# Kernel tuning notes

Hardware: AMD Instinct MI355X
Metric: run time of the kernel (lower is better)

## Reference

```python
import jax, jax.numpy as jnp
import numpy as np

B, N, KS = 4, 4096, 16  # ks = int(k * random_rate) = int(20 * 0.8)
EPS = 1e-5


def bn_relu(x):
    # training-mode BatchNorm (stats over all dims but channel=last) + ReLU
    ax = tuple(range(x.ndim - 1))
    m = x.mean(ax, keepdims=True)
    v = x.var(ax, keepdims=True)
    return jax.nn.relu((x - m) * jax.lax.rsqrt(v + EPS))


def knn_idx(points, ks):
    # points: [B,N,3] -> neighbor indices [B,N,ks] (self included)
    sq = jnp.sum(points * points, -1)
    d2 = sq[:, :, None] + sq[:, None, :] - 2.0 * jnp.einsum('bnd,bmd->bnm', points, points)
    _, idx = jax.lax.top_k(-d2, ks)
    return idx


def gather(f, idx):
    # f: [B,N,C], idx: [B,N,k] -> [B,N,k,C]
    return jax.vmap(lambda ff, ii: ff[ii])(f, idx)


def edge_conv(feat, idx, W, pts=None):
    # EdgeConv: concat(x_i, x_j - x_i [, p_j - p_i]) -> 1x1 conv -> BN+ReLU -> max_k
    nb = gather(feat, idx)                       # [B,N,k,C]
    c = feat[:, :, None, :]
    e = jnp.concatenate([jnp.broadcast_to(c, nb.shape), nb - c], -1)
    if pts is not None:
        e = jnp.concatenate([e, gather(pts, idx) - pts[:, :, None, :]], -1)
    h = jnp.einsum('bnkc,cd->bnkd', e, W)
    return bn_relu(h).max(2)                     # [B,N,out]


def graph_conv(feat, idx, W):
    agg = gather(feat, idx).max(2)               # [B,N,C]
    return bn_relu(agg @ W)


def forward(data, W_fc, b_fc, W1, W2, W3, W4, W5, W6, W10, W11, W12, W13):
    pts = data[..., :3]
    idx = knn_idx(pts, KS)                       # [B,N,KS]
    x0 = bn_relu(data @ W_fc + b_fc)             # fc_start + bn_start, [B,N,64]
    x = edge_conv(x0, idx, W1, pts=pts)          # spFEM 64 -> 256 (edge dim 131)
    x = graph_conv(x, idx, W2)                   # 256 -> 64
    x = graph_conv(x, idx, W3)                   # 64 -> 64
    x1 = x
    x = edge_conv(x, idx, W4)                    # FEM 64 -> 256 (edge dim 128)
    x = graph_conv(x, idx, W5)                   # 256 -> 64
    x = graph_conv(x, idx, W6)                   # 64 -> 64
    x2 = x
    # (conv7..conv90 produce x3/x4 which the head never consumes -> skipped)
    x12 = jnp.concatenate([x1, x2], -1)          # [B,N,128]
    h = bn_relu(x12 @ W10)                       # conv10: 128 -> 1024
    g = h.max(1)                                 # global max pool, [B,1024]
    cat = jnp.concatenate([jnp.broadcast_to(g[:, None, :], (B, N, 1024)), x1, x2], -1)  # [B,N,1152]
    h = bn_relu(cat @ W11)                       # conv11: 1152 -> 512
    h = bn_relu(h @ W12)                         # conv12: 512 -> 256
    out = h @ W13                                # conv13: 256 -> 13 (dropout = identity in eval)
    return out.transpose(0, 2, 1)                # [B,13,N]


def setup_inputs() -> dict:
    key = jax.random.key(0)
    ks = jax.random.split(key, 16)
    w = lambda k, *s: jax.random.normal(k, s, jnp.float32) * 0.05
    return {
        'data': jax.random.normal(ks[0], (B, N, 9), jnp.float32),
        'W_fc': w(ks[1], 9, 64), 'b_fc': jnp.zeros((64,), jnp.float32),
        'W1': w(ks[2], 131, 256),   # 2*64 + 3 (sp variant adds p_j - p_i)
        'W2': w(ks[3], 256, 64), 'W3': w(ks[4], 64, 64),
        'W4': w(ks[5], 128, 256),   # 2*64
        'W5': w(ks[6], 256, 64), 'W6': w(ks[7], 64, 64),
        'W10': w(ks[8], 128, 1024), 'W11': w(ks[9], 1152, 512),
        'W12': w(ks[10], 512, 256), 'W13': w(ks[11], 256, 13),
    }


def reference(data, W_fc, b_fc, W1, W2, W3, W4, W5, W6, W10, W11, W12, W13):
    return forward(data, W_fc, b_fc, W1, W2, W3, W4, W5, W6, W10, W11, W12, W13)
```

## Files before the change

kernel.cpp:

```cpp
#include <hip/hip_runtime.h>
#include <hip/hip_bf16.h>
#include <float.h>

static constexpr int BB  = 4;
static constexpr int NN  = 4096;
static constexpr int KSN = 16;
static constexpr int RN  = BB * NN;
#define EPSBN 1e-5f

typedef __attribute__((ext_vector_type(8))) short short8;
typedef __attribute__((ext_vector_type(4))) short short4v;
typedef __attribute__((ext_vector_type(4))) float f32x4;

__device__ inline unsigned short f2bf(float f) {
  union { float f; unsigned u; } v; v.f = f;
  unsigned r = v.u + 0x7FFF + ((v.u >> 16) & 1);
  return (unsigned short)(r >> 16);
}
__device__ inline float bf2f(unsigned short h) {
  union { unsigned u; float f; } v; v.u = ((unsigned)h) << 16; return v.f;
}

__global__ __launch_bounds__(256) void prepgram_kernel(const float* __restrict__ data,
                                                       float4* __restrict__ pack,
                                                       float* __restrict__ partials) {
  const int t = blockIdx.x * 256 + threadIdx.x;
  const int lane = threadIdx.x & 63, wave = threadIdx.x >> 6;
  __shared__ float red[4][54];
  float d[9];
#pragma unroll
  for (int k = 0; k < 9; ++k) d[k] = data[(size_t)t * 9 + k];
  pack[t] = make_float4(d[0], d[1], d[2], fmaf(d[2], d[2], fmaf(d[1], d[1], d[0] * d[0])));
  int p = 0;
#pragma unroll
  for (int i = 0; i < 9; ++i) {
    float v = d[i];
#pragma unroll
    for (int mv = 1; mv < 64; mv <<= 1) v += __shfl_xor(v, mv);
    if (lane == 0) red[wave][p] = v;
    ++p;
  }
#pragma unroll
  for (int i = 0; i < 9; ++i)
#pragma unroll
    for (int j = i; j < 9; ++j) {
      float v = d[i] * d[j];
#pragma unroll
      for (int mv = 1; mv < 64; mv <<= 1) v += __shfl_xor(v, mv);
      if (lane == 0) red[wave][p] = v;
      ++p;
    }
  __syncthreads();
  if (threadIdx.x < 54)
    partials[blockIdx.x * 54 + threadIdx.x] =
        red[0][threadIdx.x] + red[1][threadIdx.x] + red[2][threadIdx.x] + red[3][threadIdx.x];
}

__global__ void fcstats_kernel(const float* __restrict__ partials,
                               const float* __restrict__ W, const float* __restrict__ bias,
                               float* __restrict__ S0) {
  __shared__ float g[54];
  const int t = threadIdx.x;
  if (t < 54) {
    float s = 0.f;
    for (int b = 0; b < 64; ++b) s += partials[b * 54 + t];
    g[t] = s;
  }
  __syncthreads();
  float w[9];
#pragma unroll
  for (int k = 0; k < 9; ++k) w[k] = W[k * 64 + t];
  float b = bias[t];
  float dotw = 0.f;
#pragma unroll
  for (int k = 0; k < 9; ++k) dotw = fmaf(g[k], w[k], dotw);
  float s2 = 0.f;
  int p = 9;
#pragma unroll
  for (int i = 0; i < 9; ++i)
#pragma unroll
    for (int j = i; j < 9; ++j) {
      float gij = g[p++];
      s2 = fmaf(gij * ((i == j) ? 1.f : 2.f), w[i] * w[j], s2);
    }
  s2 += 2.f * b * dotw + (float)RN * b * b;
  S0[t] = dotw + (float)RN * b;
  S0[64 + t] = s2;
}

__global__ __launch_bounds__(256) void fc_bnpack_kernel(
    const float* __restrict__ data, const float* __restrict__ W,
    const float* __restrict__ bias, const float* __restrict__ stats,
    unsigned short* __restrict__ hi, unsigned short* __restrict__ lo) {
  const int t = blockIdx.x * 256 + threadIdx.x;
  const int r = t >> 6, c = t & 63;
  const float* dr = data + (size_t)r * 9;
  float acc = bias[c];
#pragma unroll
  for (int k = 0; k < 9; ++k) acc = fmaf(dr[k], W[k * 64 + c], acc);
  const float inv = 1.0f / RN;
  float m = stats[c] * inv;
  float v = fmaxf(stats[64 + c] * inv - m * m, 0.0f);
  float x = fmaxf((acc - m) * rsqrtf(v + EPSBN), 0.0f);
  unsigned short h = f2bf(x);
  hi[t] = h; lo[t] = f2bf(x - bf2f(h));
}

__device__ inline void wpack_one(const float* __restrict__ W, unsigned short* __restrict__ wh,
                                 unsigned short* __restrict__ wl, int t, int lgC, int NK) {
  int k = t >> lgC, c = t & ((1 << lgC) - 1);
  float v = W[t];
  int ct = c >> 4, cl = c & 15, ks = k >> 5, kl = k & 31;
  int dst = ((ct * NK + ks) * 64 + (((kl >> 3) << 4) | cl)) * 8 + (kl & 7);
  unsigned short h = f2bf(v);
  wh[dst] = h; wl[dst] = f2bf(v - bf2f(h));
}
__device__ inline void diffpack_one(const float* __restrict__ W, unsigned short* __restrict__ wh,
                                    unsigned short* __restrict__ wl, int t) {
  int k = t >> 8, cc = t & 255;
  float v = W[k * 256 + cc] - W[(64 + k) * 256 + cc];
  int ct = cc >> 4, cl = cc & 15, ks = k >> 5, kl = k & 31;
  int dst = ((ct * 2 + ks) * 64 + (((kl >> 3) << 4) | cl)) * 8 + (kl & 7);
  unsigned short h = f2bf(v);
  wh[dst] = h; wl[dst] = f2bf(v - bf2f(h));
}

__global__ __launch_bounds__(256) void megaprep_kernel(
    const float* __restrict__ W1, const float* __restrict__ W4,
    const float* __restrict__ W2, const float* __restrict__ W3,
    const float* __restrict__ W5, const float* __restrict__ W6,
    const float* __restrict__ W10, const float* __restrict__ W11, const float* __restrict__ W12,
    unsigned short* __restrict__ W1mh, unsigned short* __restrict__ W1ml, float4* __restrict__ W1bt,
    unsigned short* __restrict__ W4mh, unsigned short* __restrict__ W4ml,
    unsigned short* __restrict__ W1ph, unsigned short* __restrict__ W1pl,
    unsigned short* __restrict__ W4ph, unsigned short* __restrict__ W4pl,
    unsigned short* __restrict__ W2h, unsigned short* __restrict__ W2l,
    unsigned short* __restrict__ W3h, unsigned short* __restrict__ W3l,
    unsigned short* __restrict__ W5h, unsigned short* __restrict__ W5l,
    unsigned short* __restrict__ W6h, unsigned short* __restrict__ W6l,
    unsigned short* __restrict__ W10h, unsigned short* __restrict__ W10l,
    unsigned short* __restrict__ W11h, unsigned short* __restrict__ W11l,
    unsigned short* __restrict__ W12h, unsigned short* __restrict__ W12l) {
  const int blk = blockIdx.x;
  if (blk < 64) {
    int t = blk * 256 + threadIdx.x;
    int k = t >> 8, cc = t & 255;
    float w1mid = W1[(64 + k) * 256 + cc];
    unsigned short h1 = f2bf(w1mid);
    W1mh[cc * 64 + k] = h1;
    W1ml[cc * 64 + k] = f2bf(w1mid - bf2f(h1));
    float w4mid = W4[(64 + k) * 256 + cc];
    unsigned short h4 = f2bf(w4mid);
    W4mh[cc * 64 + k] = h4;
    W4ml[cc * 64 + k] = f2bf(w4mid - bf2f(h4));
    if (t < 256) W1bt[t] = make_float4(W1[128 * 256 + t], W1[129 * 256 + t], W1[130 * 256 + t], 0.f);
  } else if (blk < 128) {
    diffpack_one(W1, W1ph, W1pl, (blk - 64) * 256 + threadIdx.x);
  } else if (blk < 192) {
    diffpack_one(W4, W4ph, W4pl, (blk - 128) * 256 + threadIdx.x);
  } else if (blk < 256) {
    wpack_one(W2, W2h, W2l, (blk - 192) * 256 + threadIdx.x, 6, 8);
  } else if (blk < 272) {
    wpack_one(W3, W3h, W3l, (blk - 256) * 256 + threadIdx.x, 6, 2);
  } else if (blk < 336) {
    wpack_one(W5, W5h, W5l, (blk - 272) * 256 + threadIdx.x, 6, 8);
  } else if (blk < 352) {
    wpack_one(W6, W6h, W6l, (blk - 336) * 256 + threadIdx.x, 6, 2);
  } else if (blk < 864) {
    wpack_one(W10, W10h, W10l, (blk - 352) * 256 + threadIdx.x, 10, 4);
  } else if (blk < 3168) {
    wpack_one(W11, W11h, W11l, (blk - 864) * 256 + threadIdx.x, 9, 36);
  } else {
    wpack_one(W12, W12h, W12l, (blk - 3168) * 256 + threadIdx.x, 8, 16);
  }
}

__global__ void pack_x12_kernel(const float* __restrict__ x1, const float* __restrict__ x2,
                                const float* __restrict__ S6,
                                unsigned short* __restrict__ ph, unsigned short* __restrict__ pl) {
  int t = blockIdx.x * 256 + threadIdx.x;
  int r = t >> 7, k = t & 127;
  float v;
  if (k < 64) {
    v = x1[(size_t)r * 64 + k];
  } else {
    int c = k - 64;
    const float inv = 1.0f / RN;
    float m = S6[c] * inv;
    float var = fmaxf(S6[64 + c] * inv - m * m, 0.f);
    v = fmaxf((x2[(size_t)r * 64 + c] - m) * rsqrtf(var + EPSBN), 0.f);
  }
  int rt = r >> 4, rl = r & 15, ks = k >> 5, kl = k & 31;
  int dst = ((rt * 4 + ks) * 64 + (((kl >> 3) << 4) | rl)) * 8 + (kl & 7);
  unsigned short h = f2bf(v);
  ph[dst] = h; pl[dst] = f2bf(v - bf2f(h));
}

__global__ void bn_pack_kernel(const float* __restrict__ buf, const float* __restrict__ stats,
                               unsigned short* __restrict__ ph, unsigned short* __restrict__ pl) {
  int t = blockIdx.x * 256 + threadIdx.x;
  int c = t & 511, r = t >> 9;
  const float inv = 1.0f / RN;
  float m = stats[c] * inv;
  float v = fmaxf(stats[512 + c] * inv - m * m, 0.0f);
  float x = fmaxf((buf[t] - m) * rsqrtf(v + EPSBN), 0.0f);
  int rt = r >> 4, rl = r & 15, ks = c >> 5, kl = c & 31;
  int dst = ((rt * 16 + ks) * 64 + (((kl >> 3) << 4) | rl)) * 8 + (kl & 7);
  unsigned short h = f2bf(x);
  ph[dst] = h; pl[dst] = f2bf(x - bf2f(h));
}

__global__ void bn_normpack_kernel(float* __restrict__ buf, const float* __restrict__ stats,
                                   unsigned short* __restrict__ hi, unsigned short* __restrict__ lo) {
  int t = blockIdx.x * 256 + threadIdx.x;
  int c = t & 63;
  const float inv = 1.0f / RN;
  float m = stats[c] * inv;
  float v = fmaxf(stats[64 + c] * inv - m * m, 0.0f);
  float x = fmaxf((buf[t] - m) * rsqrtf(v + EPSBN), 0.0f);
  buf[t] = x;
  unsigned short h = f2bf(x);
  hi[t] = h; lo[t] = f2bf(x - bf2f(h));
}

__global__ __launch_bounds__(256) void knn_kernel(const float4* __restrict__ pack,
                                                  int* __restrict__ idx) {
  const int lane = threadIdx.x & 63;
  const int p = blockIdx.x * 4 + (threadIdx.x >> 6);
  const int b = p >> 12;
  const float4* __restrict__ pb = pack + ((size_t)b << 12);
  const float4 me = pack[p];
  unsigned long long m0 = ~0ull, m1 = ~0ull, m2 = ~0ull, m3 = ~0ull;
  float f3 = __uint_as_float(0x7FFFFFFFu);
#pragma unroll 8
  for (int s = 0; s < 64; ++s) {
    const float4 q = pb[s * 64 + lane];
    float d = me.w + q.w - 2.0f * fmaf(me.x, q.x, fmaf(me.y, q.y, me.z * q.z));
    if (!(d > f3)) {
      unsigned ub = __float_as_uint(d);
      ub = (ub & 0x80000000u) ? ~ub : (ub | 0x80000000u);
      unsigned long long k = ((unsigned long long)ub << 12) | (unsigned)(s * 64 + lane);
      if (k < m3) {
        bool l0 = k < m0;  unsigned long long t0 = l0 ? m0 : k;  m0 = l0 ? k : m0;
        bool l1 = t0 < m1; unsigned long long t1 = l1 ? m1 : t0; m1 = l1 ? t0 : m1;
        bool l2 = t1 < m2; unsigned long long t2 = l2 ? m2 : t1; m2 = l2 ? t1 : m2;
        m3 = (t2 < m3) ? t2 : m3;
        unsigned u3 = (unsigned)(m3 >> 12);
        u3 = (u3 & 0x80000000u) ? (u3 & 0x7FFFFFFFu) : ~u3;
        f3 = __uint_as_float(u3);
      }
    }
  }
  for (int pass = 0; pass < 16; ++pass) {
    unsigned long long w = m0;
#pragma unroll
    for (int mv = 1; mv < 64; mv <<= 1) {
      unsigned long long o = __shfl_xor(w, mv);
      w = (o < w) ? o : w;
    }
    if (lane == pass) idx[(p << 4) + pass] = (int)(w & 0xFFFull);
    if (m0 == w) { m0 = m1; m1 = m2; m2 = m3; m3 = ~0ull; }
    if (pass < 15 && __any(m0 == ~0ull)) {
      if (m0 == ~0ull) {
        m1 = ~0ull; m2 = ~0ull; m3 = ~0ull;
        float g3 = __uint_as_float(0x7FFFFFFFu);
#pragma unroll 8
        for (int s = 0; s < 64; ++s) {
          const float4 q = pb[s * 64 + lane];
          float d = me.w + q.w - 2.0f * fmaf(me.x, q.x, fmaf(me.y, q.y, me.z * q.z));
          if (!(d > g3)) {
            unsigned ub = __float_as_uint(d);
            ub = (ub & 0x80000000u) ? ~ub : (ub | 0x80000000u);
            unsigned long long k = ((unsigned long long)ub << 12) | (unsigned)(s * 64 + lane);
            k = (k > w) ? k : ~0ull;
            if (k < m3) {
              bool l0 = k < m0;  unsigned long long t0 = l0 ? m0 : k;  m0 = l0 ? k : m0;
              bool l1 = t0 < m1; unsigned long long t1 = l1 ? m1 : t0; m1 = l1 ? t0 : m1;
              bool l2 = t1 < m2; unsigned long long t2 = l2 ? m2 : t1; m2 = l2 ? t1 : m2;
              m3 = (t2 < m3) ? t2 : m3;
              unsigned u3 = (unsigned)(m3 >> 12);
              u3 = (u3 & 0x80000000u) ? (u3 & 0x7FFFFFFFu) : ~u3;
              g3 = __uint_as_float(u3);
            }
          }
        }
      }
    }
  }
}

template <bool HAS_PTS>
__global__ __launch_bounds__(256) void edge_mfma_kernel(
    const unsigned short* __restrict__ Xh, const unsigned short* __restrict__ Xl,
    const int* __restrict__ idx,
    const float4* __restrict__ pack,
    const unsigned short* __restrict__ Wmh, const unsigned short* __restrict__ Wml,
    const float4* __restrict__ Wbt, const float* __restrict__ basemat,
    float* __restrict__ out, float* __restrict__ stats) {
  const int wave = threadIdx.x >> 6;
  const int lane = threadIdx.x & 63;
  const int pg   = blockIdx.x;
  const int c0   = wave << 6;
  const int cl   = lane & 15;
  const int kg   = (lane >> 4) << 3;
  const int bat  = pg >> 8;
  const int pbase = bat << 12;
  const int ib   = pg << 8;

  short8 bh[4][2], blo[4][2];
#pragma unroll
  for (int q = 0; q < 4; ++q) {
    const unsigned short* wp = Wmh + (size_t)(c0 + q * 16 + cl) * 64 + kg;
    bh[q][0] = *(const short8*)wp; bh[q][1] = *(const short8*)(wp + 32);
    const unsigned short* wq = Wml + (size_t)(c0 + q * 16 + cl) * 64 + kg;
    blo[q][0] = *(const short8*)wq; blo[q][1] = *(const short8*)(wq + 32);
  }
  float4 wb[4];
  if (HAS_PTS) {
#pragma unroll
    for (int q = 0; q < 4; ++q) wb[q] = Wbt[c0 + q * 16 + cl];
  }
  float P1[4] = {0.f, 0.f, 0.f, 0.f}, P2[4] = {0.f, 0.f, 0.f, 0.f};
  float PCx[4] = {0.f, 0.f, 0.f, 0.f};
  float PB1[4] = {0.f, 0.f, 0.f, 0.f}, PB2[4] = {0.f, 0.f, 0.f, 0.f};

  int jn = idx[ib + 16 + cl];
  int j0 = idx[ib + cl];
  size_t ro = ((size_t)(pbase | j0) << 6) + kg;
  short8 a0h = *(const short8*)(Xh + ro);
  short8 a1h = *(const short8*)(Xh + ro + 32);
  short8 a0l = *(const short8*)(Xl + ro);
  short8 a1l = *(const short8*)(Xl + ro + 32);

  for (int pp = 0; pp < 16; ++pp) {
    const int p = (pg << 4) | pp;
    int jf = 0;
    if (pp < 14) jf = idx[ib + ((pp + 2) << 4) + cl];
    short8 n0h, n1h, n0l, n1l;
    if (pp < 15) {
      size_t rn = ((size_t)(pbase | jn) << 6) + kg;
      n0h = *(const short8*)(Xh + rn);
      n1h = *(const short8*)(Xh + rn + 32);
      n0l = *(const short8*)(Xl + rn);
      n1l = *(const short8*)(Xl + rn + 32);
    }
    float dx0, dy0, dz0, dx1, dy1, dz1, dx2, dy2, dz2, dx3, dy3, dz3;
    if (HAS_PTS) {
      const int4 j4 = *(const int4*)(idx + (p << 4) + ((lane >> 4) << 2));
      const float4 pc = pack[p];
      const float4 q0 = pack[pbase | j4.x];
      const float4 q1 = pack[pbase | j4.y];
      const float4 q2 = pack[pbase | j4.z];
      const float4 q3 = pack[pbase | j4.w];
      dx0 = q0.x - pc.x; dy0 = q0.y - pc.y; dz0 = q0.z - pc.z;
      dx1 = q1.x - pc.x; dy1 = q1.y - pc.y; dz1 = q1.z - pc.z;
      dx2 = q2.x - pc.x; dy2 = q2.y - pc.y; dz2 = q2.z - pc.z;
      dx3 = q3.x - pc.x; dy3 = q3.y - pc.y; dz3 = q3.z - pc.z;
    }
    f32x4 acc[4];
#pragma unroll
    for (int q = 0; q < 4; ++q) {
      acc[q][0] = 0.f; acc[q][1] = 0.f; acc[q][2] = 0.f; acc[q][3] = 0.f;
    }
#pragma unroll
    for (int q = 0; q < 4; ++q) {
      acc[q] = __builtin_amdgcn_mfma_f32_16x16x32_bf16(a0l, bh[q][0], acc[q], 0, 0, 0);
      acc[q] = __builtin_amdgcn_mfma_f32_16x16x32_bf16(a1l, bh[q][1], acc[q], 0, 0, 0);
      acc[q] = __builtin_amdgcn_mfma_f32_16x16x32_bf16(a0h, blo[q][0], acc[q], 0, 0, 0);
      acc[q] = __builtin_amdgcn_mfma_f32_16x16x32_bf16(a1h, blo[q][1], acc[q], 0, 0, 0);
      acc[q] = __builtin_amdgcn_mfma_f32_16x16x32_bf16(a0h, bh[q][0], acc[q], 0, 0, 0);
      acc[q] = __builtin_amdgcn_mfma_f32_16x16x32_bf16(a1h, bh[q][1], acc[q], 0, 0, 0);
    }
    if (HAS_PTS) {
#pragma unroll
      for (int q = 0; q < 4; ++q) {
        acc[q][0] += dx0 * wb[q].x + dy0 * wb[q].y + dz0 * wb[q].z;
        acc[q][1] += dx1 * wb[q].x + dy1 * wb[q].y + dz1 * wb[q].z;
        acc[q][2] += dx2 * wb[q].x + dy2 * wb[q].y + dz2 * wb[q].z;
        acc[q][3] += dx3 * wb[q].x + dy3 * wb[q].y + dz3 * wb[q].z;
      }
    }
#pragma unroll
    for (int q = 0; q < 4; ++q) {
      float s1p = acc[q][0] + acc[q][1] + acc[q][2] + acc[q][3];
      float s2p = acc[q][0] * acc[q][0] + acc[q][1] * acc[q][1]
                + acc[q][2] * acc[q][2] + acc[q][3] * acc[q][3];
      float mx = fmaxf(fmaxf(acc[q][0], acc[q][1]), fmaxf(acc[q][2], acc[q][3]));
      mx = fmaxf(mx, __shfl_xor(mx, 16));
      mx = fmaxf(mx, __shfl_xor(mx, 32));
      float bb = basemat[(size_t)p * 256 + c0 + q * 16 + cl];
      if (lane < 16) out[(size_t)p * 256 + c0 + q * 16 + cl] = mx + bb;
      P1[q] += s1p;
      P2[q] += s2p;
      PCx[q] = fmaf(bb, s1p, PCx[q]);
      PB1[q] += bb;
      PB2[q] = fmaf(bb, bb, PB2[q]);
    }
    a0h = n0h; a1h = n1h; a0l = n0l; a1l = n1l;
    jn = jf;
  }
#pragma unroll
  for (int q = 0; q < 4; ++q) {
    float p1 = P1[q]; p1 += __shfl_xor(p1, 16); p1 += __shfl_xor(p1, 32);
    float p2 = P2[q]; p2 += __shfl_xor(p2, 16); p2 += __shfl_xor(p2, 32);
    float pc = PCx[q]; pc += __shfl_xor(pc, 16); pc += __shfl_xor(pc, 32);
    if (lane < 16) {
      atomicAdd(&stats[c0 + q * 16 + lane], p1 + 16.f * PB1[q]);
      atomicAdd(&stats[256 + c0 + q * 16 + lane], p2 + 2.f * pc + 16.f * PB2[q]);
    }
  }
}

template <int LGC>
__global__ __launch_bounds__(256) void agg_pack_kernel(
    const float* __restrict__ X, const int* __restrict__ idx,
    const float* __restrict__ stats, float inv_cnt,
    unsigned short* __restrict__ ph, unsigned short* __restrict__ pl) {
  const int C = 1 << LGC;
  const int xcd = blockIdx.x & 7, bat = xcd >> 1;
  const int j = ((blockIdx.x >> 3) << 1) | (xcd & 1);
  const int rows_per_block = 256 >> (LGC - 2);
  const int r = bat * 4096 + j * rows_per_block + (threadIdx.x >> (LGC - 2));
  const int cq = threadIdx.x & ((C >> 2) - 1);
  const int base = bat << 12;
  const int* ip = idx + (size_t)r * KSN;
  float4 mx = make_float4(-FLT_MAX, -FLT_MAX, -FLT_MAX, -FLT_MAX);
#pragma unroll
  for (int k = 0; k < KSN; ++k) {
    int jj = ip[k];
    const float4 v = *reinterpret_cast<const float4*>(X + (size_t)(base + jj) * C + cq * 4);
    mx.x = fmaxf(mx.x, v.x); mx.y = fmaxf(mx.y, v.y);
    mx.z = fmaxf(mx.z, v.z); mx.w = fmaxf(mx.w, v.w);
  }
  const int c = cq * 4;
  const float4 sa = *reinterpret_cast<const float4*>(stats + c);
  const float4 sb = *reinterpret_cast<const float4*>(stats + C + c);
  float m0 = sa.x * inv_cnt, m1 = sa.y * inv_cnt, m2 = sa.z * inv_cnt, m3 = sa.w * inv_cnt;
  float o0 = fmaxf((mx.x - m0) * rsqrtf(fmaxf(sb.x * inv_cnt - m0 * m0, 0.f) + EPSBN), 0.f);
  float o1 = fmaxf((mx.y - m1) * rsqrtf(fmaxf(sb.y * inv_cnt - m1 * m1, 0.f) + EPSBN), 0.f);
  float o2 = fmaxf((mx.z - m2) * rsqrtf(fmaxf(sb.z * inv_cnt - m2 * m2, 0.f) + EPSBN), 0.f);
  float o3 = fmaxf((mx.w - m3) * rsqrtf(fmaxf(sb.w * inv_cnt - m3 * m3, 0.f) + EPSBN), 0.f);
  short4v H, L;
  H.x = (short)f2bf(o0); L.x = (short)f2bf(o0 - bf2f((unsigned short)H.x));
  H.y = (short)f2bf(o1); L.y = (short)f2bf(o1 - bf2f((unsigned short)H.y));
  H.z = (short)f2bf(o2); L.z = (short)f2bf(o2 - bf2f((unsigned short)H.z));
  H.w = (short)f2bf(o3); L.w = (short)f2bf(o3 - bf2f((unsigned short)H.w));
  const int NK = C >> 5;
  const int rt = r >> 4, rl = r & 15, ks = c >> 5, kl = c & 31;
  const size_t dst = (((size_t)rt * NK + ks) * 64 + (((kl >> 3) << 4) | rl)) * 8 + (kl & 7);
  *(short4v*)(ph + dst) = H;
  *(short4v*)(pl + dst) = L;
}

template <int AMODE, bool DOMAX>
__global__ __launch_bounds__(256) void gemm_mfma_kernel(
    const unsigned short* __restrict__ Ah, const unsigned short* __restrict__ Al,
    const unsigned short* __restrict__ gh, const unsigned short* __restrict__ gl,
    const unsigned short* __restrict__ Wh, const unsigned short* __restrict__ Wl,
    float* __restrict__ Y, float* __restrict__ pmax, float* __restrict__ stats,
    int K, int C) {
  __shared__ float red1[4][64], red2[4][64], redm[4][64];
  const int wave = threadIdx.x >> 6, lane = threadIdx.x & 63;
  const int rtb = blockIdx.x * 16 + wave * 4;
  const int c0  = blockIdx.y * 64;
  const int ct0 = blockIdx.y * 4;
  const int NK  = K >> 5;
  const int KP  = (AMODE == 3) ? 4 : NK;
  const int bat = blockIdx.x >> 4;
  f32x4 acc[4][4];
#pragma unroll
  for (int r = 0; r < 4; ++r)
#pragma unroll
    for (int cc = 0; cc < 4; ++cc) {
      acc[r][cc][0] = 0.f; acc[r][cc][1] = 0.f; acc[r][cc][2] = 0.f; acc[r][cc][3] = 0.f;
    }
  const int lhalf = (lane >> 4) << 3;
  for (int ks = 0; ks < NK; ++ks) {
    short8 ah[4], al[4];
    if (AMODE == 3 && ks < 32) {
      const int go = bat * 1024 + ks * 32 + lhalf;
      short8 gav = *(const short8*)(gh + go);
      short8 galv = *(const short8*)(gl + go);
#pragma unroll
      for (int r = 0; r < 4; ++r) { ah[r] = gav; al[r] = galv; }
    } else if (AMODE == 1) {
#pragma unroll
      for (int r = 0; r < 4; ++r) {
        const size_t aoff = ((size_t)((rtb + r) * 16 + (lane & 15))) * 64 + ks * 32 + lhalf;
        ah[r] = *(const short8*)(Ah + aoff);
        al[r] = *(const short8*)(Al + aoff);
      }
    } else {
      const int ksp = (AMODE == 3) ? ks - 32 : ks;
#pragma unroll
      for (int r = 0; r < 4; ++r) {
        const size_t aoff = (((size_t)(rtb + r) * KP + ksp) * 64 + lane) * 8;
        ah[r] = *(const short8*)(Ah + aoff);
        al[r] = *(const short8*)(Al + aoff);
      }
    }
#pragma unroll
    for (int cc = 0; cc < 4; ++cc) {
      const size_t woff = (((size_t)(ct0 + cc) * NK + ks) * 64 + lane) * 8;
      short8 bh = *(const short8*)(Wh + woff);
      short8 bl = *(const short8*)(Wl + woff);
#pragma unroll
      for (int r = 0; r < 4; ++r) {
        acc[r][cc] = __builtin_amdgcn_mfma_f32_16x16x32_bf16(al[r], bh, acc[r][cc], 0, 0, 0);
        acc[r][cc] = __builtin_amdgcn_mfma_f32_16x16x32_bf16(ah[r], bl, acc[r][cc], 0, 0, 0);
        acc[r][cc] = __builtin_amdgcn_mfma_f32_16x16x32_bf16(ah[r], bh, acc[r][cc], 0, 0, 0);
      }
    }
  }
#pragma unroll
  for (int cc = 0; cc < 4; ++cc) {
    float s1 = 0.f, s2 = 0.f, mm = -FLT_MAX;
#pragma unroll
    for (int r = 0; r < 4; ++r) {
      if (!DOMAX) {
#pragma unroll
        for (int i = 0; i < 4; ++i)
          Y[(size_t)((rtb + r) * 16 + ((lane >> 4) << 2) + i) * C + c0 + cc * 16 + (lane & 15)] = acc[r][cc][i];
      }
#pragma unroll
      for (int i = 0; i < 4; ++i) {
        float v = acc[r][cc][i];
        s1 += v; s2 = fmaf(v, v, s2); mm = fmaxf(mm, v);
      }
    }
    s1 += __shfl_xor(s1, 16); s1 += __shfl_xor(s1, 32);
    s2 += __shfl_xor(s2, 16); s2 += __shfl_xor(s2, 32);
    mm = fmaxf(mm, __shfl_xor(mm, 16)); mm = fmaxf(mm, __shfl_xor(mm, 32));
    if (lane < 16) {
      red1[wave][cc * 16 + lane] = s1;
      red2[wave][cc * 16 + lane] = s2;
      if (DOMAX) redm[wave][cc * 16 + lane] = mm;
    }
  }
  __syncthreads();
  if (threadIdx.x < 64) {
    const int t = threadIdx.x;
    float a = red1[0][t] + red1[1][t] + red1[2][t] + red1[3][t];
    float b = red2[0][t] + red2[1][t] + red2[2][t] + red2[3][t];
    atomicAdd(&stats[c0 + t], a);
    atomicAdd(&stats[C + c0 + t], b);
    if (DOMAX) {
      float mm = fmaxf(fmaxf(redm[0][t], redm[1][t]), fmaxf(redm[2][t], redm[3][t]));
      pmax[(size_t)blockIdx.x * C + c0 + t] = mm;
    }
  }
}

__global__ void fin_g_kernel(const float* __restrict__ pmax, const float* __restrict__ stats,
                             unsigned short* __restrict__ gh, unsigned short* __restrict__ gl) {
  int t = blockIdx.x * 256 + threadIdx.x;
  int b = t >> 10, c = t & 1023;
  const float inv = 1.0f / 16384.0f;
  float m = stats[c] * inv;
  float v = fmaxf(stats[1024 + c] * inv - m * m, 0.0f);
  float rs = rsqrtf(v + EPSBN);
  float mx = -FLT_MAX;
  for (int s = 0; s < 16; ++s) mx = fmaxf(mx, pmax[(size_t)(b * 16 + s) * 1024 + c]);
  float val = fmaxf((mx - m) * rs, 0.0f);
  unsigned short h = f2bf(val);
  gh[t] = h; gl[t] = f2bf(val - bf2f(h));
}

__global__ __launch_bounds__(256) void final13_kernel(const float* __restrict__ h,
                                                      const float* __restrict__ S9,
                                                      const float* __restrict__ W,
                                                      float* __restrict__ out) {
  __shared__ float wl[256 * 13];
  __shared__ float ms[256], rs[256];
  const int t = threadIdx.x;
  {
    const float inv = 1.0f / RN;
    float m = S9[t] * inv;
    float v = fmaxf(S9[256 + t] * inv - m * m, 0.0f);
    ms[t] = m; rs[t] = rsqrtf(v + EPSBN);
#pragma unroll
    for (int i = 0; i < 13; ++i) wl[t * 13 + i] = W[t * 13 + i];
  }
  __syncthreads();
  const int r = blockIdx.x * 16 + (t >> 4);
  const int c = t & 15;
  const int ci = (c < 13) ? c : 0;
  const float* hr = h + (size_t)r * 256;
  float acc = 0.0f;
  for (int k = 0; k < 256; ++k) {
    float x = fmaxf((hr[k] - ms[k]) * rs[k], 0.0f);
    acc = fmaf(x, wl[k * 13 + ci], acc);
  }
  if (c < 13) {
    int b = r >> 12, n = r & 4095;
    out[(size_t)b * 13 * NN + (size_t)c * NN + n] = acc;
  }
}

extern "C" void kernel_launch(void* const* d_in, const int* in_sizes, int n_in,
                              void* d_out, int out_size, void* d_ws, size_t ws_size,
                              hipStream_t stream) {
  (void)in_sizes; (void)n_in; (void)out_size; (void)ws_size;
  const float* data = (const float*)d_in[0];
  const float* W_fc = (const float*)d_in[1];
  const float* b_fc = (const float*)d_in[2];
  const float* W1   = (const float*)d_in[3];
  const float* W2   = (const float*)d_in[4];
  const float* W3   = (const float*)d_in[5];
  const float* W4   = (const float*)d_in[6];
  const float* W5   = (const float*)d_in[7];
  const float* W6   = (const float*)d_in[8];
  const float* W10  = (const float*)d_in[9];
  const float* W11  = (const float*)d_in[10];
  const float* W12  = (const float*)d_in[11];
  const float* W13  = (const float*)d_in[12];
  float* out = (float*)d_out;

  float* ws  = (float*)d_ws;
  int*   idx = (int*)d_ws;
  size_t o = 262144;
  float* x0   = ws + o; o += (size_t)RN * 64;
  float* x1v  = ws + o; o += (size_t)RN * 64;
  float* x2v  = ws + o; o += (size_t)RN * 64;
  float* bufA = ws + o; o += (size_t)RN * 256;
  float* bufB = ws + o; o += (size_t)RN * 256;
  float* bufC = ws + o; o += (size_t)RN * 64;
  float* pmax = ws + o; o += (size_t)64 * 1024;
  float* h11  = ws + o; o += (size_t)RN * 512;
  float* h12  = ws + o; o += (size_t)RN * 256;
  float* stats = ws + o; o += 8192;
  float4* pack = (float4*)(ws + o); o += (size_t)RN * 4;
  unsigned short* xbh = (unsigned short*)(ws + o); o += (size_t)RN * 32;
  unsigned short* xbl = (unsigned short*)(ws + o); o += (size_t)RN * 32;
  unsigned short* W1mh = (unsigned short*)(ws + o); o += 8192;
  unsigned short* W1ml = (unsigned short*)(ws + o); o += 8192;
  unsigned short* W4mh = (unsigned short*)(ws + o); o += 8192;
  unsigned short* W4ml = (unsigned short*)(ws + o); o += 8192;
  float4* W1bt = (float4*)(ws + o); o += 1024;
  unsigned short* W10h = (unsigned short*)(ws + o); o += 65536;
  unsigned short* W10l = (unsigned short*)(ws + o); o += 65536;
  unsigned short* W11h = (unsigned short*)(ws + o); o += 294912;
  unsigned short* W11l = (unsigned short*)(ws + o); o += 294912;
  unsigned short* W12h = (unsigned short*)(ws + o); o += 65536;
  unsigned short* W12l = (unsigned short*)(ws + o); o += 65536;
  unsigned short* gh   = (unsigned short*)(ws + o); o += 2048;
  unsigned short* gl   = (unsigned short*)(ws + o); o += 2048;
  unsigned short* W1ph = (unsigned short*)(ws + o); o += 8192;
  unsigned short* W1pl = (unsigned short*)(ws + o); o += 8192;
  unsigned short* W4ph = (unsigned short*)(ws + o); o += 8192;
  unsigned short* W4pl = (unsigned short*)(ws + o); o += 8192;
  unsigned short* W2h  = (unsigned short*)(ws + o); o += 8192;
  unsigned short* W2l  = (unsigned short*)(ws + o); o += 8192;
  unsigned short* W3h  = (unsigned short*)(ws + o); o += 2048;
  unsigned short* W3l  = (unsigned short*)(ws + o); o += 2048;
  unsigned short* W5h  = (unsigned short*)(ws + o); o += 8192;
  unsigned short* W5l  = (unsigned short*)(ws + o); o += 8192;
  unsigned short* W6h  = (unsigned short*)(ws + o); o += 2048;
  unsigned short* W6l  = (unsigned short*)(ws + o); o += 2048;
  float* gpart = ws + o; o += 64 * 54;
  unsigned short* x12h = (unsigned short*)bufC;
  unsigned short* x12l = (unsigned short*)x0;
  unsigned short* h11h = (unsigned short*)bufA;
  unsigned short* h11l = (unsigned short*)bufB;
  unsigned short* aggh = (unsigned short*)h11;
  unsigned short* aggl = (unsigned short*)h11 + (size_t)RN * 256;

  float* S0 = stats;
  float* S1 = stats + 128;
  float* S2 = stats + 640;
  float* S3 = stats + 768;
  float* S4 = stats + 896;
  float* S5 = stats + 1408;
  float* S6 = stats + 1536;
  float* S7 = stats + 1664;
  float* S8 = stats + 3712;
  float* S9 = stats + 4736;
  float* Sd = stats + 5248;

  hipMemsetAsync(stats, 0, 8192 * sizeof(float), stream);

  prepgram_kernel<<<64, 256, 0, stream>>>(data, pack, gpart);
  megaprep_kernel<<<3680, 256, 0, stream>>>(
      W1, W4, W2, W3, W5, W6, W10, W11, W12,
      W1mh, W1ml, W1bt, W4mh, W4ml,
      W1ph, W1pl, W4ph, W4pl, W2h, W2l, W3h, W3l, W5h, W5l, W6h, W6l,
      W10h, W10l, W11h, W11l, W12h, W12l);
  knn_kernel<<<RN / 4, 256, 0, stream>>>(pack, idx);
  fcstats_kernel<<<1, 64, 0, stream>>>(gpart, W_fc, b_fc, S0);
  fc_bnpack_kernel<<<RN * 64 / 256, 256, 0, stream>>>(data, W_fc, b_fc, S0, xbh, xbl);

  gemm_mfma_kernel<1, false><<<dim3(64, 4), 256, 0, stream>>>(
      xbh, xbl, nullptr, nullptr, W1ph, W1pl, bufB, nullptr, Sd, 64, 256);
  edge_mfma_kernel<true><<<1024, 256, 0, stream>>>(xbh, xbl, idx, pack, W1mh, W1ml, W1bt, bufB, bufA, S1);

  agg_pack_kernel<8><<<4096, 256, 0, stream>>>(bufA, idx, S1, 1.0f / (RN * 16), aggh, aggl);
  gemm_mfma_kernel<0, false><<<dim3(64, 1), 256, 0, stream>>>(
      aggh, aggl, nullptr, nullptr, W2h, W2l, bufC, nullptr, S2, 256, 64);

  agg_pack_kernel<6><<<1024, 256, 0, stream>>>(bufC, idx, S2, 1.0f / RN, aggh, aggl);
  gemm_mfma_kernel<0, false><<<dim3(64, 1), 256, 0, stream>>>(
      aggh, aggl, nullptr, nullptr, W3h, W3l, x1v, nullptr, S3, 64, 64);
  bn_normpack_kernel<<<RN * 64 / 256, 256, 0, stream>>>(x1v, S3, xbh, xbl);

  gemm_mfma_kernel<1, false><<<dim3(64, 4), 256, 0, stream>>>(
      xbh, xbl, nullptr, nullptr, W4ph, W4pl, bufB, nullptr, Sd, 64, 256);
  edge_mfma_kernel<false><<<1024, 256, 0, stream>>>(xbh, xbl, idx, pack, W4mh, W4ml, nullptr, bufB, bufA, S4);

  agg_pack_kernel<8><<<4096, 256, 0, stream>>>(bufA, idx, S4, 1.0f / (RN * 16), aggh, aggl);
  gemm_mfma_kernel<0, false><<<dim3(64, 1), 256, 0, stream>>>(
      aggh, aggl, nullptr, nullptr, W5h, W5l, bufC, nullptr, S5, 256, 64);

  agg_pack_kernel<6><<<1024, 256, 0, stream>>>(bufC, idx, S5, 1.0f / RN, aggh, aggl);
  gemm_mfma_kernel<0, false><<<dim3(64, 1), 256, 0, stream>>>(
      aggh, aggl, nullptr, nullptr, W6h, W6l, x2v, nullptr, S6, 64, 64);

  pack_x12_kernel<<<RN * 128 / 256, 256, 0, stream>>>(x1v, x2v, S6, x12h, x12l);

  gemm_mfma_kernel<0, true><<<dim3(64, 16), 256, 0, stream>>>(
      x12h, x12l, nullptr, nullptr, W10h, W10l, nullptr, pmax, S7, 128, 1024);
  fin_g_kernel<<<16, 256, 0, stream>>>(pmax, S7, gh, gl);

  gemm_mfma_kernel<3, false><<<dim3(64, 8), 256, 0, stream>>>(
      x12h, x12l, gh, gl, W11h, W11l, h11, nullptr, S8, 1152, 512);
  bn_pack_kernel<<<RN * 512 / 256, 256, 0, stream>>>(h11, S8, h11h, h11l);

  gemm_mfma_kernel<0, false><<<dim3(64, 4), 256, 0, stream>>>(
      h11h, h11l, nullptr, nullptr, W12h, W12l, h12, nullptr, S9, 512, 256);

  final13_kernel<<<RN / 16, 256, 0, stream>>>(h12, S9, W13, out);
}
```

Measured before the change: 613.9 us.

## Fold global feature into per-batch W11 bias and merge knn/fc/prep kernels

The global-pooled feature is constant across points, so its 1024x512 contribution to conv11 is computed once per batch by a small kernel and added as a bias. The conv11 GEMM then contracts only the 128 per-point channels, and only that slice of W11 is packed. The knn, fc+BN pack and weight-prep kernels are merged into a single launch, and the knn tie-break reduction is reworked to shuffle 32-bit keys with a ballot fallback. The price is an fp32 serial dot product in gb11, and the knn loop loses its early-reject threshold check.

New measurement: 598.2 us. 1.03x faster.

```diff
diff --git a/kernel.cpp b/kernel.cpp
--- a/kernel.cpp
+++ b/kernel.cpp
@@ -88,24 +88,6 @@
   S0[64 + t] = s2;
 }
 
-__global__ __launch_bounds__(256) void fc_bnpack_kernel(
-    const float* __restrict__ data, const float* __restrict__ W,
-    const float* __restrict__ bias, const float* __restrict__ stats,
-    unsigned short* __restrict__ hi, unsigned short* __restrict__ lo) {
-  const int t = blockIdx.x * 256 + threadIdx.x;
-  const int r = t >> 6, c = t & 63;
-  const float* dr = data + (size_t)r * 9;
-  float acc = bias[c];
-#pragma unroll
-  for (int k = 0; k < 9; ++k) acc = fmaf(dr[k], W[k * 64 + c], acc);
-  const float inv = 1.0f / RN;
-  float m = stats[c] * inv;
-  float v = fmaxf(stats[64 + c] * inv - m * m, 0.0f);
-  float x = fmaxf((acc - m) * rsqrtf(v + EPSBN), 0.0f);
-  unsigned short h = f2bf(x);
-  hi[t] = h; lo[t] = f2bf(x - bf2f(h));
-}
-
 __device__ inline void wpack_one(const float* __restrict__ W, unsigned short* __restrict__ wh,
                                  unsigned short* __restrict__ wl, int t, int lgC, int NK) {
   int k = t >> lgC, c = t & ((1 << lgC) - 1);
@@ -125,7 +107,11 @@
   wh[dst] = h; wl[dst] = f2bf(v - bf2f(h));
 }
 
-__global__ __launch_bounds__(256) void megaprep_kernel(
+__global__ __launch_bounds__(256) void mega_kernel(
+    const float4* __restrict__ pack, int* __restrict__ idx,
+    const float* __restrict__ data, const float* __restrict__ W_fc,
+    const float* __restrict__ b_fc, const float* __restrict__ S0,
+    unsigned short* __restrict__ xbh, unsigned short* __restrict__ xbl,
     const float* __restrict__ W1, const float* __restrict__ W4,
     const float* __restrict__ W2, const float* __restrict__ W3,
     const float* __restrict__ W5, const float* __restrict__ W6,
@@ -139,39 +125,121 @@
     unsigned short* __restrict__ W5h, unsigned short* __restrict__ W5l,
     unsigned short* __restrict__ W6h, unsigned short* __restrict__ W6l,
     unsigned short* __restrict__ W10h, unsigned short* __restrict__ W10l,
-    unsigned short* __restrict__ W11h, unsigned short* __restrict__ W11l,
+    unsigned short* __restrict__ W11xh, unsigned short* __restrict__ W11xl,
     unsigned short* __restrict__ W12h, unsigned short* __restrict__ W12l) {
   const int blk = blockIdx.x;
-  if (blk < 64) {
-    int t = blk * 256 + threadIdx.x;
-    int k = t >> 8, cc = t & 255;
-    float w1mid = W1[(64 + k) * 256 + cc];
-    unsigned short h1 = f2bf(w1mid);
-    W1mh[cc * 64 + k] = h1;
-    W1ml[cc * 64 + k] = f2bf(w1mid - bf2f(h1));
-    float w4mid = W4[(64 + k) * 256 + cc];
-    unsigned short h4 = f2bf(w4mid);
-    W4mh[cc * 64 + k] = h4;
-    W4ml[cc * 64 + k] = f2bf(w4mid - bf2f(h4));
-    if (t < 256) W1bt[t] = make_float4(W1[128 * 256 + t], W1[129 * 256 + t], W1[130 * 256 + t], 0.f);
-  } else if (blk < 128) {
-    diffpack_one(W1, W1ph, W1pl, (blk - 64) * 256 + threadIdx.x);
-  } else if (blk < 192) {
-    diffpack_one(W4, W4ph, W4pl, (blk - 128) * 256 + threadIdx.x);
-  } else if (blk < 256) {
-    wpack_one(W2, W2h, W2l, (blk - 192) * 256 + threadIdx.x, 6, 8);
-  } else if (blk < 272) {
-    wpack_one(W3, W3h, W3l, (blk - 256) * 256 + threadIdx.x, 6, 2);
-  } else if (blk < 336) {
-    wpack_one(W5, W5h, W5l, (blk - 272) * 256 + threadIdx.x, 6, 8);
-  } else if (blk < 352) {
-    wpack_one(W6, W6h, W6l, (blk - 336) * 256 + threadIdx.x, 6, 2);
-  } else if (blk < 864) {
-    wpack_one(W10, W10h, W10l, (blk - 352) * 256 + threadIdx.x, 10, 4);
-  } else if (blk < 3168) {
-    wpack_one(W11, W11h, W11l, (blk - 864) * 256 + threadIdx.x, 9, 36);
+  if (blk < 4096) {
+    const int lane = threadIdx.x & 63;
+    const int p = blk * 4 + (threadIdx.x >> 6);
+    const int b = p >> 12;
+    const float4* __restrict__ pb = pack + ((size_t)b << 12);
+    const float4 me = pack[p];
+    unsigned long long m0 = ~0ull, m1 = ~0ull, m2 = ~0ull, m3 = ~0ull;
+#pragma unroll 8
+    for (int s = 0; s < 64; ++s) {
+      const float4 q = pb[s * 64 + lane];
+      float d = me.w + q.w - 2.0f * fmaf(me.x, q.x, fmaf(me.y, q.y, me.z * q.z));
+      unsigned ub = __float_as_uint(d);
+      ub = (ub & 0x80000000u) ? ~ub : (ub | 0x80000000u);
+      unsigned long long k = ((unsigned long long)ub << 12) | (unsigned)(s * 64 + lane);
+      if (k < m3) {
+        bool l0 = k < m0;  unsigned long long t0 = l0 ? m0 : k;  m0 = l0 ? k : m0;
+        bool l1 = t0 < m1; unsigned long long t1 = l1 ? m1 : t0; m1 = l1 ? t0 : m1;
+        bool l2 = t1 < m2; unsigned long long t2 = l2 ? m2 : t1; m2 = l2 ? t1 : m2;
+        m3 = (t2 < m3) ? t2 : m3;
+      }
+    }
+    for (int pass = 0; pass < 16; ++pass) {
+      unsigned d0 = (unsigned)(m0 >> 12);
+      unsigned w32 = d0;
+#pragma unroll
+      for (int mv = 1; mv < 64; mv <<= 1) {
+        unsigned o = __shfl_xor(w32, mv);
+        w32 = (o < w32) ? o : w32;
+      }
+      unsigned long long ball = __ballot(d0 == w32);
+      unsigned widx;
+      if (__popcll(ball) == 1) {
+        widx = __shfl((unsigned)(m0 & 0xFFFull), (int)(__ffsll((long long)ball) - 1));
+      } else {
+        unsigned cand = (d0 == w32) ? (unsigned)(m0 & 0xFFFull) : 0xFFFFFFFFu;
+#pragma unroll
+        for (int mv = 1; mv < 64; mv <<= 1) {
+          unsigned o = __shfl_xor(cand, mv);
+          cand = (o < cand) ? o : cand;
+        }
+        widx = cand;
+      }
+      const unsigned long long w = ((unsigned long long)w32 << 12) | widx;
+      if (lane == pass) idx[(p << 4) + pass] = (int)widx;
+      if (m0 == w) { m0 = m1; m1 = m2; m2 = m3; m3 = ~0ull; }
+      if (pass < 15 && __any(m0 == ~0ull)) {
+        if (m0 == ~0ull) {
+          m1 = ~0ull; m2 = ~0ull; m3 = ~0ull;
+#pragma unroll 8
+          for (int s = 0; s < 64; ++s) {
+            const float4 q = pb[s * 64 + lane];
+            float d = me.w + q.w - 2.0f * fmaf(me.x, q.x, fmaf(me.y, q.y, me.z * q.z));
+            unsigned ub = __float_as_uint(d);
+            ub = (ub & 0x80000000u) ? ~ub : (ub | 0x80000000u);
+            unsigned long long k = ((unsigned long long)ub << 12) | (unsigned)(s * 64 + lane);
+            k = (k > w) ? k : ~0ull;
+            if (k < m3) {
+              bool l0 = k < m0;  unsigned long long t0 = l0 ? m0 : k;  m0 = l0 ? k : m0;
+              bool l1 = t0 < m1; unsigned long long t1 = l1 ? m1 : t0; m1 = l1 ? t0 : m1;
+              bool l2 = t1 < m2; unsigned long long t2 = l2 ? m2 : t1; m2 = l2 ? t1 : m2;
+              m3 = (t2 < m3) ? t2 : m3;
+            }
+          }
+        }
+      }
+    }
+  } else if (blk < 8192) {
+    const int t = (blk - 4096) * 256 + threadIdx.x;
+    const int r = t >> 6, c = t & 63;
+    const float* dr = data + (size_t)r * 9;
+    float acc = b_fc[c];
+#pragma unroll
+    for (int k = 0; k < 9; ++k) acc = fmaf(dr[k], W_fc[k * 64 + c], acc);
+    const float inv = 1.0f / RN;
+    float m = S0[c] * inv;
+    float v = fmaxf(S0[64 + c] * inv - m * m, 0.0f);
+    float x = fmaxf((acc - m) * rsqrtf(v + EPSBN), 0.0f);
+    unsigned short h = f2bf(x);
+    xbh[t] = h; xbl[t] = f2bf(x - bf2f(h));
   } else {
-    wpack_one(W12, W12h, W12l, (blk - 3168) * 256 + threadIdx.x, 8, 16);
+    const int mb = blk - 8192;
+    if (mb < 64) {
+      int t = mb * 256 + threadIdx.x;
+      int k = t >> 8, cc = t & 255;
+      float w1mid = W1[(64 + k) * 256 + cc];
+      unsigned short h1 = f2bf(w1mid);
+      W1mh[cc * 64 + k] = h1;
+      W1ml[cc * 64 + k] = f2bf(w1mid - bf2f(h1));
+      float w4mid = W4[(64 + k) * 256 + cc];
+      unsigned short h4 = f2bf(w4mid);
+      W4mh[cc * 64 + k] = h4;
+      W4ml[cc * 64 + k] = f2bf(w4mid - bf2f(h4));
+      if (t < 256) W1bt[t] = make_float4(W1[128 * 256 + t], W1[129 * 256 + t], W1[130 * 256 + t], 0.f);
+    } else if (mb < 128) {
+      diffpack_one(W1, W1ph, W1pl, (mb - 64) * 256 + threadIdx.x);
+    } else if (mb < 192) {
+      diffpack_one(W4, W4ph, W4pl, (mb - 128) * 256 + threadIdx.x);
+    } else if (mb < 256) {
+      wpack_one(W2, W2h, W2l, (mb - 192) * 256 + threadIdx.x, 6, 8);
+    } else if (mb < 272) {
+      wpack_one(W3, W3h, W3l, (mb - 256) * 256 + threadIdx.x, 6, 2);
+    } else if (mb < 336) {
+      wpack_one(W5, W5h, W5l, (mb - 272) * 256 + threadIdx.x, 6, 8);
+    } else if (mb < 352) {
+      wpack_one(W6, W6h, W6l, (mb - 336) * 256 + threadIdx.x, 6, 2);
+    } else if (mb < 864) {
+      wpack_one(W10, W10h, W10l, (mb - 352) * 256 + threadIdx.x, 10, 4);
+    } else if (mb < 1120) {
+      wpack_one(W11 + 1024 * 512, W11xh, W11xl, (mb - 864) * 256 + threadIdx.x, 9, 4);
+    } else {
+      wpack_one(W12, W12h, W12l, (mb - 1120) * 256 + threadIdx.x, 8, 16);
+    }
   }
 }
 
@@ -221,72 +289,6 @@
   buf[t] = x;
   unsigned short h = f2bf(x);
   hi[t] = h; lo[t] = f2bf(x - bf2f(h));
-}
-
-__global__ __launch_bounds__(256) void knn_kernel(const float4* __restrict__ pack,
-                                                  int* __restrict__ idx) {
-  const int lane = threadIdx.x & 63;
-  const int p = blockIdx.x * 4 + (threadIdx.x >> 6);
-  const int b = p >> 12;
-  const float4* __restrict__ pb = pack + ((size_t)b << 12);
-  const float4 me = pack[p];
-  unsigned long long m0 = ~0ull, m1 = ~0ull, m2 = ~0ull, m3 = ~0ull;
-  float f3 = __uint_as_float(0x7FFFFFFFu);
-#pragma unroll 8
-  for (int s = 0; s < 64; ++s) {
-    const float4 q = pb[s * 64 + lane];
-    float d = me.w + q.w - 2.0f * fmaf(me.x, q.x, fmaf(me.y, q.y, me.z * q.z));
-    if (!(d > f3)) {
-      unsigned ub = __float_as_uint(d);
-      ub = (ub & 0x80000000u) ? ~ub : (ub | 0x80000000u);
-      unsigned long long k = ((unsigned long long)ub << 12) | (unsigned)(s * 64 + lane);
-      if (k < m3) {
-        bool l0 = k < m0;  unsigned long long t0 = l0 ? m0 : k;  m0 = l0 ? k : m0;
-        bool l1 = t0 < m1; unsigned long long t1 = l1 ? m1 : t0; m1 = l1 ? t0 : m1;
-        bool l2 = t1 < m2; unsigned long long t2 = l2 ? m2 : t1; m2 = l2 ? t1 : m2;
-        m3 = (t2 < m3) ? t2 : m3;
-        unsigned u3 = (unsigned)(m3 >> 12);
-        u3 = (u3 & 0x80000000u) ? (u3 & 0x7FFFFFFFu) : ~u3;
-        f3 = __uint_as_float(u3);
-      }
-    }
-  }
-  for (int pass = 0; pass < 16; ++pass) {
-    unsigned long long w = m0;
-#pragma unroll
-    for (int mv = 1; mv < 64; mv <<= 1) {
-      unsigned long long o = __shfl_xor(w, mv);
-      w = (o < w) ? o : w;
-    }
-    if (lane == pass) idx[(p << 4) + pass] = (int)(w & 0xFFFull);
-    if (m0 == w) { m0 = m1; m1 = m2; m2 = m3; m3 = ~0ull; }
-    if (pass < 15 && __any(m0 == ~0ull)) {
-      if (m0 == ~0ull) {
-        m1 = ~0ull; m2 = ~0ull; m3 = ~0ull;
-        float g3 = __uint_as_float(0x7FFFFFFFu);
-#pragma unroll 8
-        for (int s = 0; s < 64; ++s) {
-          const float4 q = pb[s * 64 + lane];
-          float d = me.w + q.w - 2.0f * fmaf(me.x, q.x, fmaf(me.y, q.y, me.z * q.z));
-          if (!(d > g3)) {
-            unsigned ub = __float_as_uint(d);
-            ub = (ub & 0x80000000u) ? ~ub : (ub | 0x80000000u);
-            unsigned long long k = ((unsigned long long)ub << 12) | (unsigned)(s * 64 + lane);
-            k = (k > w) ? k : ~0ull;
-            if (k < m3) {
-              bool l0 = k < m0;  unsigned long long t0 = l0 ? m0 : k;  m0 = l0 ? k : m0;
-              bool l1 = t0 < m1; unsigned long long t1 = l1 ? m1 : t0; m1 = l1 ? t0 : m1;
-              bool l2 = t1 < m2; unsigned long long t2 = l2 ? m2 : t1; m2 = l2 ? t1 : m2;
-              m3 = (t2 < m3) ? t2 : m3;
-              unsigned u3 = (unsigned)(m3 >> 12);
-              u3 = (u3 & 0x80000000u) ? (u3 & 0x7FFFFFFFu) : ~u3;
-              g3 = __uint_as_float(u3);
-            }
-          }
-        }
-      }
-    }
-  }
 }
 
 template <bool HAS_PTS>
@@ -452,12 +454,12 @@
   *(short4v*)(pl + dst) = L;
 }
 
-template <int AMODE, bool DOMAX>
+template <int AMODE, bool DOMAX, bool BIAS>
 __global__ __launch_bounds__(256) void gemm_mfma_kernel(
     const unsigned short* __restrict__ Ah, const unsigned short* __restrict__ Al,
-    const unsigned short* __restrict__ gh, const unsigned short* __restrict__ gl,
     const unsigned short* __restrict__ Wh, const unsigned short* __restrict__ Wl,
     float* __restrict__ Y, float* __restrict__ pmax, float* __restrict__ stats,
+    const float* __restrict__ gbias,
     int K, int C) {
   __shared__ float red1[4][64], red2[4][64], redm[4][64];
   const int wave = threadIdx.x >> 6, lane = threadIdx.x & 63;
@@ -465,7 +467,6 @@
   const int c0  = blockIdx.y * 64;
   const int ct0 = blockIdx.y * 4;
   const int NK  = K >> 5;
-  const int KP  = (AMODE == 3) ? 4 : NK;
   const int bat = blockIdx.x >> 4;
   f32x4 acc[4][4];
 #pragma unroll
@@ -477,13 +478,7 @@
   const int lhalf = (lane >> 4) << 3;
   for (int ks = 0; ks < NK; ++ks) {
     short8 ah[4], al[4];
-    if (AMODE == 3 && ks < 32) {
-      const int go = bat * 1024 + ks * 32 + lhalf;
-      short8 gav = *(const short8*)(gh + go);
-      short8 galv = *(const short8*)(gl + go);
-#pragma unroll
-      for (int r = 0; r < 4; ++r) { ah[r] = gav; al[r] = galv; }
-    } else if (AMODE == 1) {
+    if (AMODE == 1) {
 #pragma unroll
       for (int r = 0; r < 4; ++r) {
         const size_t aoff = ((size_t)((rtb + r) * 16 + (lane & 15))) * 64 + ks * 32 + lhalf;
@@ -491,10 +486,9 @@
         al[r] = *(const short8*)(Al + aoff);
       }
     } else {
-      const int ksp = (AMODE == 3) ? ks - 32 : ks;
 #pragma unroll
       for (int r = 0; r < 4; ++r) {
-        const size_t aoff = (((size_t)(rtb + r) * KP + ksp) * 64 + lane) * 8;
+        const size_t aoff = (((size_t)(rtb + r) * NK + ks) * 64 + lane) * 8;
         ah[r] = *(const short8*)(Ah + aoff);
         al[r] = *(const short8*)(Al + aoff);
       }
@@ -514,17 +508,16 @@
   }
 #pragma unroll
   for (int cc = 0; cc < 4; ++cc) {
+    float bv = 0.f;
+    if (BIAS) bv = gbias[(size_t)bat * C + c0 + cc * 16 + (lane & 15)];
     float s1 = 0.f, s2 = 0.f, mm = -FLT_MAX;
 #pragma unroll
     for (int r = 0; r < 4; ++r) {
-      if (!DOMAX) {
-#pragma unroll
-        for (int i = 0; i < 4; ++i)
-          Y[(size_t)((rtb + r) * 16 + ((lane >> 4) << 2) + i) * C + c0 + cc * 16 + (lane & 15)] = acc[r][cc][i];
-      }
 #pragma unroll
       for (int i = 0; i < 4; ++i) {
-        float v = acc[r][cc][i];
+        float v = acc[r][cc][i] + bv;
+        if (!DOMAX)
+          Y[(size_t)((rtb + r) * 16 + ((lane >> 4) << 2) + i) * C + c0 + cc * 16 + (lane & 15)] = v;
         s1 += v; s2 = fmaf(v, v, s2); mm = fmaxf(mm, v);
       }
     }
@@ -552,7 +545,7 @@
 }
 
 __global__ void fin_g_kernel(const float* __restrict__ pmax, const float* __restrict__ stats,
-                             unsigned short* __restrict__ gh, unsigned short* __restrict__ gl) {
+                             float* __restrict__ gf) {
   int t = blockIdx.x * 256 + threadIdx.x;
   int b = t >> 10, c = t & 1023;
   const float inv = 1.0f / 16384.0f;
@@ -561,9 +554,19 @@
   float rs = rsqrtf(v + EPSBN);
   float mx = -FLT_MAX;
   for (int s = 0; s < 16; ++s) mx = fmaxf(mx, pmax[(size_t)(b * 16 + s) * 1024 + c]);
-  float val = fmaxf((mx - m) * rs, 0.0f);
-  unsigned short h = f2bf(val);
-  gh[t] = h; gl[t] = f2bf(val - bf2f(h));
+  gf[t] = fmaxf((mx - m) * rs, 0.0f);
+}
+
+__global__ __launch_bounds__(256) void gb11_kernel(const float* __restrict__ gf,
+                                                   const float* __restrict__ W11,
+                                                   float* __restrict__ gb) {
+  int t = blockIdx.x * 256 + threadIdx.x;
+  int b = t >> 9, c = t & 511;
+  const float* g = gf + b * 1024;
+  float acc = 0.f;
+#pragma unroll 8
+  for (int k = 0; k < 1024; ++k) acc = fmaf(g[k], W11[(size_t)k * 512 + c], acc);
+  gb[t] = acc;
 }
 
 __global__ __launch_bounds__(256) void final13_kernel(const float* __restrict__ h,
@@ -639,12 +642,12 @@
   float4* W1bt = (float4*)(ws + o); o += 1024;
   unsigned short* W10h = (unsigned short*)(ws + o); o += 65536;
   unsigned short* W10l = (unsigned short*)(ws + o); o += 65536;
-  unsigned short* W11h = (unsigned short*)(ws + o); o += 294912;
-  unsigned short* W11l = (unsigned short*)(ws + o); o += 294912;
+  unsigned short* W11xh = (unsigned short*)(ws + o); o += 32768;
+  unsigned short* W11xl = (unsigned short*)(ws + o); o += 32768;
   unsigned short* W12h = (unsigned short*)(ws + o); o += 65536;
   unsigned short* W12l = (unsigned short*)(ws + o); o += 65536;
-  unsigned short* gh   = (unsigned short*)(ws + o); o += 2048;
-  unsigned short* gl   = (unsigned short*)(ws + o); o += 2048;
+  float* gf = ws + o; o += 4096;
+  float* gb = ws + o; o += 2048;
   unsigned short* W1ph = (unsigned short*)(ws + o); o += 8192;
   unsigned short* W1pl = (unsigned short*)(ws + o); o += 8192;
   unsigned short* W4ph = (unsigned short*)(ws + o); o += 8192;
@@ -680,52 +683,53 @@
   hipMemsetAsync(stats, 0, 8192 * sizeof(float), stream);
 
   prepgram_kernel<<<64, 256, 0, stream>>>(data, pack, gpart);
-  megaprep_kernel<<<3680, 256, 0, stream>>>(
+  fcstats_kernel<<<1, 64, 0, stream>>>(gpart, W_fc, b_fc, S0);
+
+  mega_kernel<<<9824, 256, 0, stream>>>(
+      pack, idx, data, W_fc, b_fc, S0, xbh, xbl,
       W1, W4, W2, W3, W5, W6, W10, W11, W12,
       W1mh, W1ml, W1bt, W4mh, W4ml,
       W1ph, W1pl, W4ph, W4pl, W2h, W2l, W3h, W3l, W5h, W5l, W6h, W6l,
-      W10h, W10l, W11h, W11l, W12h, W12l);
-  knn_kernel<<<RN / 4, 256, 0, stream>>>(pack, idx);
-  fcstats_kernel<<<1, 64, 0, stream>>>(gpart, W_fc, b_fc, S0);
-  fc_bnpack_kernel<<<RN * 64 / 256, 256, 0, stream>>>(data, W_fc, b_fc, S0, xbh, xbl);
-
-  gemm_mfma_kernel<1, false><<<dim3(64, 4), 256, 0, stream>>>(
-      xbh, xbl, nullptr, nullptr, W1ph, W1pl, bufB, nullptr, Sd, 64, 256);
+      W10h, W10l, W11xh, W11xl, W12h, W12l);
+
+  gemm_mfma_kernel<1, false, false><<<dim3(64, 4), 256, 0, stream>>>(
+      xbh, xbl, W1ph, W1pl, bufB, nullptr, Sd, nullptr, 64, 256);
   edge_mfma_kernel<true><<<1024, 256, 0, stream>>>(xbh, xbl, idx, pack, W1mh, W1ml, W1bt, bufB, bufA, S1);
 
   agg_pack_kernel<8><<<4096, 256, 0, stream>>>(bufA, idx, S1, 1.0f / (RN * 16), aggh, aggl);
-  gemm_mfma_kernel<0, false><<<dim3(64, 1), 256, 0, stream>>>(
-      aggh, aggl, nullptr, nullptr, W2h, W2l, bufC, nullptr, S2, 256, 64);
+  gemm_mfma_kernel<0, false, false><<<dim3(64, 1), 256, 0, stream>>>(
+      aggh, aggl, W2h, W2l, bufC, nullptr, S2, nullptr, 256, 64);
 
   agg_pack_kernel<6><<<1024, 256, 0, stream>>>(bufC, idx, S2, 1.0f / RN, aggh, aggl);
-  gemm_mfma_kernel<0, false><<<dim3(64, 1), 256, 0, stream>>>(
-      aggh, aggl, nullptr, nullptr, W3h, W3l, x1v, nullptr, S3, 64, 64);
+  gemm_mfma_kernel<0, false, false><<<dim3(64, 1), 256, 0, stream>>>(
+      aggh, aggl, W3h, W3l, x1v, nullptr, S3, nullptr, 64, 64);
   bn_normpack_kernel<<<RN * 64 / 256, 256, 0, stream>>>(x1v, S3, xbh, xbl);
 
-  gemm_mfma_kernel<1, false><<<dim3(64, 4), 256, 0, stream>>>(
-      xbh, xbl, nullptr, nullptr, W4ph, W4pl, bufB, nullptr, Sd, 64, 256);
+  gemm_mfma_kernel<1, false, false><<<dim3(64, 4), 256, 0, stream>>>(
+      xbh, xbl, W4ph, W4pl, bufB, nullptr, Sd, nullptr, 64, 256);
   edge_mfma_kernel<false><<<1024, 256, 0, stream>>>(xbh, xbl, idx, pack, W4mh, W4ml, nullptr, bufB, bufA, S4);
 
   agg_pack_kernel<8><<<4096, 256, 0, stream>>>(bufA, idx, S4, 1.0f / (RN * 16), aggh, aggl);
-  gemm_mfma_kernel<0, false><<<dim3(64, 1), 256, 0, stream>>>(
-      aggh, aggl, nullptr, nullptr, W5h, W5l, bufC, nullptr, S5, 256, 64);
+  gemm_mfma_kernel<0, false, false><<<dim3(64, 1), 256, 0, stream>>>(
+      aggh, aggl, W5h, W5l, bufC, nullptr, S5, nullptr, 256, 64);
 
   agg_pack_kernel<6><<<1024, 256, 0, stream>>>(bufC, idx, S5, 1.0f / RN, aggh, aggl);
-  gemm_mfma_kernel<0, false><<<dim3(64, 1), 256, 0, stream>>>(
-      aggh, aggl, nullptr, nullptr, W6h, W6l, x2v, nullptr, S6, 64, 64);
+  gemm_mfma_kernel<0, false, false><<<dim3(64, 1), 256, 0, stream>>>(
+      aggh, aggl, W6h, W6l, x2v, nullptr, S6, nullptr, 64, 64);
 
   pack_x12_kernel<<<RN * 128 / 256, 256, 0, stream>>>(x1v, x2v, S6, x12h, x12l);
 
-  gemm_mfma_kernel<0, true><<<dim3(64, 16), 256, 0, stream>>>(
-      x12h, x12l, nullptr, nullptr, W10h, W10l, nullptr, pmax, S7, 128, 1024);
-  fin_g_kernel<<<16, 256, 0, stream>>>(pmax, S7, gh, gl);
-
-  gemm_mfma_kernel<3, false><<<dim3(64, 8), 256, 0, stream>>>(
-      x12h, x12l, gh, gl, W11h, W11l, h11, nullptr, S8, 1152, 512);
+  gemm_mfma_kernel<0, true, false><<<dim3(64, 16), 256, 0, stream>>>(
+      x12h, x12l, W10h, W10l, nullptr, pmax, S7, nullptr, 128, 1024);
+  fin_g_kernel<<<16, 256, 0, stream>>>(pmax, S7, gf);
+
+  gb11_kernel<<<8, 256, 0, stream>>>(gf, W11, gb);
+  gemm_mfma_kernel<0, false, true><<<dim3(64, 8), 256, 0, stream>>>(
+      x12h, x12l, W11xh, W11xl, h11, nullptr, S8, gb, 128, 512);
   bn_pack_kernel<<<RN * 512 / 256, 256, 0, stream>>>(h11, S8, h11h, h11l);
 
-  gemm_mfma_kernel<0, false><<<dim3(64, 4), 256, 0, stream>>>(
-      h11h, h11l, nullptr, nullptr, W12h, W12l, h12, nullptr, S9, 512, 256);
+  gemm_mfma_kernel<0, false, false><<<dim3(64, 4), 256, 0, stream>>>(
+      h11h, h11l, W12h, W12l, h12, nullptr, S9, nullptr, 512, 256);
 
   final13_kernel<<<RN / 16, 256, 0, stream>>>(h12, S9, W13, out);
 }
```
